# Kernel optimization log

Measured on AMD Instinct MI355X. Metric: run time of the kernel, lower is better.

The kernel has to match this reference:

```python
import jax, jax.numpy as jnp
import numpy as np

D_MODEL, N_HEADS, RANK, TOPK = 1024, 16, 32, 32
D_HEAD = D_MODEL // N_HEADS


def setup_inputs() -> dict:
    key = jax.random.key(0)
    ks = jax.random.split(key, 12)
    B, L, S = 2, 2048, 2048
    sc = 0.02
    return {
        "q": jax.random.normal(ks[0], (B, L, D_MODEL), jnp.float32),
        "k": jax.random.normal(ks[1], (B, S, D_MODEL), jnp.float32),
        "v": jax.random.normal(ks[2], (B, S, D_MODEL), jnp.float32),
        "Wq": jax.random.normal(ks[3], (D_MODEL, RANK * N_HEADS), jnp.float32) * sc,
        "bq": jnp.zeros((RANK * N_HEADS,), jnp.float32),
        "Wk": jax.random.normal(ks[4], (D_MODEL, RANK * N_HEADS), jnp.float32) * sc,
        "bk": jnp.zeros((RANK * N_HEADS,), jnp.float32),
        "Wv": jax.random.normal(ks[5], (D_MODEL, D_MODEL), jnp.float32) * sc,
        "bv": jnp.zeros((D_MODEL,), jnp.float32),
        "Wo": jax.random.normal(ks[6], (D_MODEL, D_MODEL), jnp.float32) * sc,
        "bo": jnp.zeros((D_MODEL,), jnp.float32),
        "pos_bias": jnp.zeros((1, N_HEADS, 1, 1), jnp.float32),
    }


def topk_sparse(logits, k):
    # keep top-k per row, mask the rest to -inf, then softmax
    top_vals = jax.lax.top_k(logits, k)[0]          # [B,H,L,k]
    kth = top_vals[..., -1:]                        # [B,H,L,1]
    masked = jnp.where(logits >= kth, logits, -jnp.inf)
    return jax.nn.softmax(masked, axis=-1)


def reference(q, k, v, Wq, bq, Wk, bk, Wv, bv, Wo, bo, pos_bias):
    B, L, _ = q.shape
    S = k.shape[1]
    Q = (q @ Wq + bq).reshape(B, L, N_HEADS, RANK).transpose(0, 2, 1, 3)   # [B,H,L,r]
    K = (k @ Wk + bk).reshape(B, S, N_HEADS, RANK).transpose(0, 2, 1, 3)   # [B,H,S,r]
    V = (v @ Wv + bv).reshape(B, S, N_HEADS, D_HEAD).transpose(0, 2, 1, 3)  # [B,H,S,d]
    scores = jnp.einsum('bhlr,bhsr->bhls', Q, K) / jnp.sqrt(jnp.float32(RANK))
    scores = scores + pos_bias
    attn = topk_sparse(scores, TOPK)                # [B,H,L,S]
    out = jnp.einsum('bhls,bhsd->bhld', attn, V)    # [B,H,L,d]
    out = out.transpose(0, 2, 1, 3).reshape(B, L, D_MODEL)
    return out @ Wo + bo
```

## Files before the change

kernel.cpp:

```cpp
#include <hip/hip_runtime.h>
#include <hip/hip_bf16.h>
#include <cstdint>

constexpr int B  = 2;
constexpr int L  = 2048;
constexpr int S  = 2048;
constexpr int DM = 1024;
constexpr int H  = 16;
constexpr int R  = 32;
constexpr int DH = 64;
constexpr int TOPK = 32;
constexpr int SELCAP = 36;
constexpr float SCALE = 0.17677669529663687f;


using short8 = __attribute__((ext_vector_type(8))) short;
using f32x4  = __attribute__((ext_vector_type(4))) float;

__device__ __forceinline__ unsigned short bf16_rne(float x) {
    unsigned int u = __float_as_uint(x);
    unsigned int r = u + 0x7FFFu + ((u >> 16) & 1u);
    return (unsigned short)(r >> 16);
}
__device__ __forceinline__ float bf16_up(unsigned short h) {
    return __uint_as_float((unsigned int)h << 16);
}
__device__ __forceinline__ float inv_sortable(unsigned int uu) {
    unsigned int sg2 = (unsigned int)(((int)uu) >> 31);
    return __uint_as_float(uu ^ (0x80000000u | ~sg2));
}

__global__ __launch_bounds__(256, 2)
void qk_proj(const float* __restrict__ Aq, const float* __restrict__ Wq_,
             const float* __restrict__ bq_, float* __restrict__ Qp,
             const float* __restrict__ Ak, const float* __restrict__ Wk_,
             const float* __restrict__ bk_, unsigned short* __restrict__ Kf,
             int M, int N, int K)
{
    const int z = blockIdx.z;
    const float* A    = z ? Ak  : Aq;
    const float* W    = z ? Wk_ : Wq_;
    const float* bias = z ? bk_ : bq_;

    __shared__ float As[16][136];
    __shared__ float Ws[16][132];

    const int t  = threadIdx.x;
    const int tx = t & 15;
    const int ty = t >> 4;
    const int m0 = blockIdx.y * 128;
    const int n0 = blockIdx.x * 128;

    float acc[8][8];
#pragma unroll
    for (int i = 0; i < 8; ++i)
#pragma unroll
        for (int j = 0; j < 8; ++j) acc[i][j] = 0.f;

    for (int kb = 0; kb < K; kb += 16) {
        __syncthreads();
#pragma unroll
        for (int it = 0; it < 2; ++it) {
            int f4  = t + it * 256;
            int row = f4 >> 2;
            int cg  = (f4 & 3) * 4;
            float4 av = *(const float4*)&A[(size_t)(m0 + row) * K + kb + cg];
            As[cg + 0][row] = av.x;
            As[cg + 1][row] = av.y;
            As[cg + 2][row] = av.z;
            As[cg + 3][row] = av.w;
        }
#pragma unroll
        for (int it = 0; it < 2; ++it) {
            int f4 = t + it * 256;
            int kk = f4 >> 5;
            int cb = (f4 & 31) * 4;
            *(float4*)&Ws[kk][cb] = *(const float4*)&W[(size_t)(kb + kk) * N + n0 + cb];
        }
        __syncthreads();
#pragma unroll
        for (int kk = 0; kk < 16; ++kk) {
            float4 a0 = *(const float4*)&As[kk][ty * 8];
            float4 a1 = *(const float4*)&As[kk][ty * 8 + 4];
            float4 w0 = *(const float4*)&Ws[kk][tx * 8];
            float4 w1 = *(const float4*)&Ws[kk][tx * 8 + 4];
            float a[8] = {a0.x, a0.y, a0.z, a0.w, a1.x, a1.y, a1.z, a1.w};
            float w[8] = {w0.x, w0.y, w0.z, w0.w, w1.x, w1.y, w1.z, w1.w};
#pragma unroll
            for (int i = 0; i < 8; ++i)
#pragma unroll
                for (int j = 0; j < 8; ++j)
                    acc[i][j] = fmaf(a[i], w[j], acc[i][j]);
        }
    }

    float4 b0 = *(const float4*)&bias[n0 + tx * 8];
    float4 b1 = *(const float4*)&bias[n0 + tx * 8 + 4];

    if (z == 0) {
#pragma unroll
        for (int i = 0; i < 8; ++i) {
            float4 o0 = make_float4((acc[i][0] + b0.x) * SCALE, (acc[i][1] + b0.y) * SCALE,
                                    (acc[i][2] + b0.z) * SCALE, (acc[i][3] + b0.w) * SCALE);
            float4 o1 = make_float4((acc[i][4] + b1.x) * SCALE, (acc[i][5] + b1.y) * SCALE,
                                    (acc[i][6] + b1.z) * SCALE, (acc[i][7] + b1.w) * SCALE);
            size_t off = (size_t)(m0 + ty * 8 + i) * N + n0 + tx * 8;
            *(float4*)&Qp[off]     = o0;
            *(float4*)&Qp[off + 4] = o1;
        }
    } else {
        float bb[8] = {b0.x, b0.y, b0.z, b0.w, b1.x, b1.y, b1.z, b1.w};
        const int h2 = (n0 + tx * 8) >> 5;
        const int l4 = ((n0 + tx * 8) & 31) >> 3;
#pragma unroll
        for (int i = 0; i < 8; ++i) {
            unsigned short hh[8], mm[8], ll[8];
#pragma unroll
            for (int j = 0; j < 8; ++j) {
                float x = acc[i][j] + bb[j];
                hh[j] = bf16_rne(x);
                float xr = x - bf16_up(hh[j]);
                mm[j] = bf16_rne(xr);
                ll[j] = bf16_rne(xr - bf16_up(mm[j]));
            }
            const int grow = m0 + ty * 8 + i;
            const int bat  = grow >> 11;
            const int key  = grow & 2047;
            const int T    = key >> 4;
            const int l15  = key & 15;
            const size_t base = (((size_t)(bat * H + h2) * 128 + T) * 1536)
                              + (size_t)(l4 * 16 + l15) * 8;
            ushort4 h0v = {hh[0], hh[1], hh[2], hh[3]}, h1v = {hh[4], hh[5], hh[6], hh[7]};
            ushort4 m0v = {mm[0], mm[1], mm[2], mm[3]}, m1v = {mm[4], mm[5], mm[6], mm[7]};
            ushort4 l0v = {ll[0], ll[1], ll[2], ll[3]}, l1v = {ll[4], ll[5], ll[6], ll[7]};
            *(ushort4*)&Kf[base]            = h0v;
            *(ushort4*)&Kf[base + 4]        = h1v;
            *(ushort4*)&Kf[base + 512]      = m0v;
            *(ushort4*)&Kf[base + 512 + 4]  = m1v;
            *(ushort4*)&Kf[base + 1024]     = l0v;
            *(ushort4*)&Kf[base + 1024 + 4] = l1v;
        }
    }
}

__global__ __launch_bounds__(256)
void transpose_split_dual(const float* __restrict__ Wv_, unsigned short* __restrict__ VhT,
                          unsigned short* __restrict__ VlT,
                          const float* __restrict__ Wo_, unsigned short* __restrict__ OhT,
                          unsigned short* __restrict__ OlT, int N, int K)
{
    const int z = blockIdx.z;
    const float* W = z ? Wo_ : Wv_;
    unsigned short* Th = z ? OhT : VhT;
    unsigned short* Tl = z ? OlT : VlT;

    __shared__ float tile[32][33];
    const int n0 = blockIdx.x * 32;
    const int k0 = blockIdx.y * 32;
    const int tx = threadIdx.x & 31;
    const int ty = threadIdx.x >> 5;

#pragma unroll
    for (int i = ty; i < 32; i += 8)
        tile[i][tx] = W[(size_t)(k0 + i) * N + n0 + tx];
    __syncthreads();
#pragma unroll
    for (int i = ty; i < 32; i += 8) {
        float x = tile[tx][i];
        unsigned short h = bf16_rne(x);
        float hf = bf16_up(h);
        unsigned short l = bf16_rne(x - hf);
        Th[(size_t)(n0 + i) * K + k0 + tx] = h;
        Tl[(size_t)(n0 + i) * K + k0 + tx] = l;
    }
}

__global__ __launch_bounds__(256, 1)
void gemm_mfma_split(const float* __restrict__ A, const unsigned short* __restrict__ Bh,
                     const unsigned short* __restrict__ Bl, const float* __restrict__ bias,
                     float* __restrict__ C, int M, int N, int K)
{
    constexpr int LDT = 56;
    __shared__ unsigned short Ah[128 * LDT];
    __shared__ unsigned short Al[128 * LDT];
    __shared__ unsigned short Wh[128 * LDT];
    __shared__ unsigned short Wl[128 * LDT];

    const int t    = threadIdx.x;
    const int lane = t & 63;
    const int w    = t >> 6;
    const int wr   = w >> 1;
    const int wc   = w & 1;
    const int l15  = lane & 15;
    const int l4   = lane >> 4;
    const int m0   = blockIdx.y * 128;
    const int n0   = blockIdx.x * 128;

    f32x4 acc[4][4];
#pragma unroll
    for (int m = 0; m < 4; ++m)
#pragma unroll
        for (int n = 0; n < 4; ++n) {
            f32x4 z = {0.f, 0.f, 0.f, 0.f};
            acc[m][n] = z;
        }

#pragma unroll 1
    for (int kb = 0; kb < K; kb += 32) {
        __syncthreads();
#pragma unroll
        for (int it = 0; it < 4; ++it) {
            int f   = t + it * 256;
            int row = f >> 3;
            int kg  = (f & 7) * 4;
            float4 av = *(const float4*)&A[(size_t)(m0 + row) * K + kb + kg];
            ushort4 hv, lv;
            hv.x = bf16_rne(av.x); lv.x = bf16_rne(av.x - bf16_up(hv.x));
            hv.y = bf16_rne(av.y); lv.y = bf16_rne(av.y - bf16_up(hv.y));
            hv.z = bf16_rne(av.z); lv.z = bf16_rne(av.z - bf16_up(hv.z));
            hv.w = bf16_rne(av.w); lv.w = bf16_rne(av.w - bf16_up(hv.w));
            *(ushort4*)&Ah[row * LDT + kg] = hv;
            *(ushort4*)&Al[row * LDT + kg] = lv;
            ushort4 bh4 = *(const ushort4*)&Bh[(size_t)(n0 + row) * K + kb + kg];
            ushort4 bl4 = *(const ushort4*)&Bl[(size_t)(n0 + row) * K + kb + kg];
            *(ushort4*)&Wh[row * LDT + kg] = bh4;
            *(ushort4*)&Wl[row * LDT + kg] = bl4;
        }
        __syncthreads();

        short8 ah[4], al[4], bh[4], bl[4];
#pragma unroll
        for (int m = 0; m < 4; ++m) {
            int row = wr * 64 + m * 16 + l15;
            ah[m] = *(short8*)&Ah[row * LDT + l4 * 8];
            al[m] = *(short8*)&Al[row * LDT + l4 * 8];
        }
#pragma unroll
        for (int n = 0; n < 4; ++n) {
            int col = wc * 64 + n * 16 + l15;
            bh[n] = *(short8*)&Wh[col * LDT + l4 * 8];
            bl[n] = *(short8*)&Wl[col * LDT + l4 * 8];
        }
#pragma unroll
        for (int m = 0; m < 4; ++m)
#pragma unroll
            for (int n = 0; n < 4; ++n)
                acc[m][n] = __builtin_amdgcn_mfma_f32_16x16x32_bf16(ah[m], bh[n], acc[m][n], 0, 0, 0);
#pragma unroll
        for (int m = 0; m < 4; ++m)
#pragma unroll
            for (int n = 0; n < 4; ++n)
                acc[m][n] = __builtin_amdgcn_mfma_f32_16x16x32_bf16(ah[m], bl[n], acc[m][n], 0, 0, 0);
#pragma unroll
        for (int m = 0; m < 4; ++m)
#pragma unroll
            for (int n = 0; n < 4; ++n)
                acc[m][n] = __builtin_amdgcn_mfma_f32_16x16x32_bf16(al[m], bh[n], acc[m][n], 0, 0, 0);
    }

#pragma unroll
    for (int m = 0; m < 4; ++m) {
        int row = m0 + wr * 64 + m * 16 + l4 * 4;
#pragma unroll
        for (int n = 0; n < 4; ++n) {
            int col = n0 + wc * 64 + n * 16 + l15;
            float bv = bias[col];
#pragma unroll
            for (int r = 0; r < 4; ++r)
                C[(size_t)(row + r) * N + col] = acc[m][n][r] + bv;
        }
    }
}

__global__ __launch_bounds__(1024, 1)
void score_select_gather(const float* __restrict__ Qp,
                         const unsigned short* __restrict__ Kf,
                         const float* __restrict__ Vp, float* __restrict__ Oh)
{
    constexpr int LDS_STRIDE = 2049;
    __shared__ float sclds[16][LDS_STRIDE];
    __shared__ unsigned short Qs[3][16][32];

    const int t    = threadIdx.x;
    const int lane = t & 63;
    const int wv   = t >> 6;

    const int wgid = blockIdx.x;
    const int xcd  = wgid & 7;
    const int jj   = wgid >> 3;
    const int bh_  = xcd + 8 * (jj >> 7);
    const int tile = jj & 127;
    const int b    = bh_ >> 4;
    const int h    = bh_ & 15;
    const int lbase = tile * 16;

    if (t < 512) {
        int row = t >> 5;
        int col = t & 31;
        float x = Qp[(size_t)(b * L + lbase + row) * (H * R) + h * R + col];
        unsigned short hh = bf16_rne(x);
        float xr = x - bf16_up(hh);
        unsigned short mm = bf16_rne(xr);
        unsigned short ll = bf16_rne(xr - bf16_up(mm));
        Qs[0][row][col] = hh;
        Qs[1][row][col] = mm;
        Qs[2][row][col] = ll;
    }
    __syncthreads();

    const int l15 = lane & 15;
    const int l4  = lane >> 4;

    const short8 ah = *(const short8*)&Qs[0][l15][l4 * 8];
    const short8 am = *(const short8*)&Qs[1][l15][l4 * 8];
    const short8 al = *(const short8*)&Qs[2][l15][l4 * 8];

    const unsigned short* kfb = Kf + (size_t)bh_ * 128 * 1536;

    auto LOADT = [&](int T0, short8& h0, short8& m0v, short8& l0v,
                     short8& h1, short8& m1v, short8& l1v) {
        const unsigned short* t0 = kfb + (size_t)T0 * 1536 + lane * 8;
        h0  = *(const short8*)(t0);
        m0v = *(const short8*)(t0 + 512);
        l0v = *(const short8*)(t0 + 1024);
        h1  = *(const short8*)(t0 + 1536);
        m1v = *(const short8*)(t0 + 2048);
        l1v = *(const short8*)(t0 + 2560);
    };
    auto COMPUTE = [&](const short8& bh0, const short8& bm0, const short8& bl0,
                       const short8& bh1, const short8& bm1, const short8& bl1, int p) {
        f32x4 acc0 = {0.f, 0.f, 0.f, 0.f};
        f32x4 acc1 = {0.f, 0.f, 0.f, 0.f};
        __builtin_amdgcn_s_setprio(1);
        acc0 = __builtin_amdgcn_mfma_f32_16x16x32_bf16(ah, bh0, acc0, 0, 0, 0);
        acc1 = __builtin_amdgcn_mfma_f32_16x16x32_bf16(ah, bh1, acc1, 0, 0, 0);
        acc0 = __builtin_amdgcn_mfma_f32_16x16x32_bf16(ah, bm0, acc0, 0, 0, 0);
        acc1 = __builtin_amdgcn_mfma_f32_16x16x32_bf16(ah, bm1, acc1, 0, 0, 0);
        acc0 = __builtin_amdgcn_mfma_f32_16x16x32_bf16(am, bh0, acc0, 0, 0, 0);
        acc1 = __builtin_amdgcn_mfma_f32_16x16x32_bf16(am, bh1, acc1, 0, 0, 0);
        acc0 = __builtin_amdgcn_mfma_f32_16x16x32_bf16(am, bm0, acc0, 0, 0, 0);
        acc1 = __builtin_amdgcn_mfma_f32_16x16x32_bf16(am, bm1, acc1, 0, 0, 0);
        acc0 = __builtin_amdgcn_mfma_f32_16x16x32_bf16(ah, bl0, acc0, 0, 0, 0);
        acc1 = __builtin_amdgcn_mfma_f32_16x16x32_bf16(ah, bl1, acc1, 0, 0, 0);
        acc0 = __builtin_amdgcn_mfma_f32_16x16x32_bf16(al, bh0, acc0, 0, 0, 0);
        acc1 = __builtin_amdgcn_mfma_f32_16x16x32_bf16(al, bh1, acc1, 0, 0, 0);
        __builtin_amdgcn_s_setprio(0);
        const int kc0 = wv * 128 + p * 32 + l15;
#pragma unroll
        for (int r = 0; r < 4; ++r) {
            sclds[l4 * 4 + r][kc0]      = acc0[r];
            sclds[l4 * 4 + r][kc0 + 16] = acc1[r];
        }
    };

    {
        short8 xh0, xm0, xl0, xh1, xm1, xl1;
        short8 yh0, ym0, yl0, yh1, ym1, yl1;
        LOADT(wv * 8 + 0, xh0, xm0, xl0, xh1, xm1, xl1);
        LOADT(wv * 8 + 2, yh0, ym0, yl0, yh1, ym1, yl1);
        COMPUTE(xh0, xm0, xl0, xh1, xm1, xl1, 0);
        LOADT(wv * 8 + 4, xh0, xm0, xl0, xh1, xm1, xl1);
        COMPUTE(yh0, ym0, yl0, yh1, ym1, yl1, 1);
        LOADT(wv * 8 + 6, yh0, ym0, yl0, yh1, ym1, yl1);
        COMPUTE(xh0, xm0, xl0, xh1, xm1, xl1, 2);
        COMPUTE(yh0, ym0, yl0, yh1, ym1, yl1, 3);
    }

    __syncthreads();

    const unsigned long long lanelt = (1ull << lane) - 1ull;
    {
        const int r = wv;

        unsigned int u[32];
#pragma unroll
        for (int j = 0; j < 32; ++j) {
            unsigned int bb  = __float_as_uint(sclds[r][j * 64 + lane]);
            unsigned int sgn = (unsigned int)(((int)bb) >> 31);
            u[j] = bb ^ (sgn | 0x80000000u);
        }

        unsigned int lmax = u[0];
#pragma unroll
        for (int j = 1; j < 32; ++j) lmax = lmax > u[j] ? lmax : u[j];
        unsigned int umx = lmax;
#pragma unroll
        for (int off = 32; off >= 1; off >>= 1) {
            unsigned int o = (unsigned int)__shfl_xor((int)umx, off, 64);
            umx = umx > o ? umx : o;
        }
        const float mx = inv_sortable(umx);

        unsigned int PM = 0;
        for (int bit = 31; bit >= 0; --bit) {
            unsigned int test = PM | (1u << bit);
            int c2 = (int)__popcll(__ballot(lmax >= test));
            if (c2 >= TOPK) {
                PM = test;
                if (c2 == TOPK) break;
            }
        }

        int cbase = 0;
#pragma unroll
        for (int j = 0; j < 32; ++j) {
            bool alive = (u[j] >= PM);
            unsigned long long m = __ballot(alive);
            if (alive) {
                int pos = cbase + (int)__popcll(m & lanelt);
                if (pos < 128) {
                    sclds[r][1024 + pos] = __uint_as_float(u[j]);
                    sclds[r][1280 + pos] = __uint_as_float((unsigned int)(j * 64 + lane));
                }
            }
            cbase += (int)__popcll(m);
        }
        const int Ncand = cbase;

        float dsum = 0.f;
        int   base = 0;

        if (Ncand <= 128) {
            const bool v0 = lane < Ncand;
            const bool v1 = 64 + lane < Ncand;
            const unsigned int c0 = v0 ? __float_as_uint(sclds[r][1024 + lane])      : 0u;
            const unsigned int c1 = v1 ? __float_as_uint(sclds[r][1024 + 64 + lane]) : 0u;
            const unsigned int i0 = v0 ? __float_as_uint(sclds[r][1280 + lane])      : 0u;
            const unsigned int i1 = v1 ? __float_as_uint(sclds[r][1280 + 64 + lane]) : 0u;

            unsigned int P = 0;
            for (int bit = 31; bit >= 0; --bit) {
                unsigned int test = P | (1u << bit);
                int c2 = (int)__popcll(__ballot(v0 && c0 >= test))
                       + (int)__popcll(__ballot(v1 && c1 >= test));
                if (c2 >= TOPK) {
                    P = test;
                    if (c2 == TOPK) break;
                }
            }

            {
                bool sel = v0 && (c0 >= P);
                unsigned long long m = __ballot(sel);
                if (sel) {
                    float e = __expf(inv_sortable(c0) - mx);
                    int pos = (int)__popcll(m & lanelt);
                    if (pos < SELCAP) {
                        sclds[r][pos]       = e;
                        sclds[r][512 + pos] = __uint_as_float(i0);
                    }
                    dsum += e;
                }
                base = (int)__popcll(m);
            }
            {
                bool sel = v1 && (c1 >= P);
                unsigned long long m = __ballot(sel);
                if (sel) {
                    float e = __expf(inv_sortable(c1) - mx);
                    int pos = base + (int)__popcll(m & lanelt);
                    if (pos < SELCAP) {
                        sclds[r][pos]       = e;
                        sclds[r][512 + pos] = __uint_as_float(i1);
                    }
                    dsum += e;
                }
                base += (int)__popcll(m);
            }
        } else {
            unsigned int P = 0;
            for (int bit = 31; bit >= 0; --bit) {
                unsigned int test = P | (1u << bit);
                int c2 = 0;
#pragma unroll
                for (int j = 0; j < 32; ++j)
                    c2 += (int)__popcll(__ballot(u[j] >= test));
                if (c2 >= TOPK) {
                    P = test;
                    if (c2 == TOPK) break;
                }
            }
#pragma unroll
            for (int j = 0; j < 32; ++j) {
                bool sel = (u[j] >= P);
                unsigned long long m = __ballot(sel);
                if (sel) {
                    float e = __expf(inv_sortable(u[j]) - mx);
                    int pos = base + (int)__popcll(m & lanelt);
                    if (pos < SELCAP) {
                        sclds[r][pos]       = e;
                        sclds[r][512 + pos] = __uint_as_float((unsigned int)(j * 64 + lane));
                    }
                    dsum += e;
                }
                base += (int)__popcll(m);
            }
        }
#pragma unroll
        for (int off = 32; off >= 1; off >>= 1)
            dsum += __shfl_xor(dsum, off, 64);

        const int cn = base < SELCAP ? base : SELCAP;
        const float inv = 1.0f / dsum;
        const float* vb = Vp + (size_t)b * S * DM + h * DH + lane;

        float a0 = 0.f, a1 = 0.f, a2 = 0.f, a3 = 0.f;
        float a4 = 0.f, a5 = 0.f, a6 = 0.f, a7 = 0.f;
        int tt = 0;
        for (; tt + 8 <= cn; tt += 8) {
            int   s0 = (int)__float_as_uint(sclds[r][512 + tt + 0]);
            int   s1 = (int)__float_as_uint(sclds[r][512 + tt + 1]);
            int   s2 = (int)__float_as_uint(sclds[r][512 + tt + 2]);
            int   s3 = (int)__float_as_uint(sclds[r][512 + tt + 3]);
            int   s4 = (int)__float_as_uint(sclds[r][512 + tt + 4]);
            int   s5 = (int)__float_as_uint(sclds[r][512 + tt + 5]);
            int   s6 = (int)__float_as_uint(sclds[r][512 + tt + 6]);
            int   s7 = (int)__float_as_uint(sclds[r][512 + tt + 7]);
            float w0 = sclds[r][tt + 0], w1 = sclds[r][tt + 1];
            float w2 = sclds[r][tt + 2], w3 = sclds[r][tt + 3];
            float w4 = sclds[r][tt + 4], w5 = sclds[r][tt + 5];
            float w6 = sclds[r][tt + 6], w7 = sclds[r][tt + 7];
            a0 = fmaf(w0, vb[(size_t)s0 * DM], a0);
            a1 = fmaf(w1, vb[(size_t)s1 * DM], a1);
            a2 = fmaf(w2, vb[(size_t)s2 * DM], a2);
            a3 = fmaf(w3, vb[(size_t)s3 * DM], a3);
            a4 = fmaf(w4, vb[(size_t)s4 * DM], a4);
            a5 = fmaf(w5, vb[(size_t)s5 * DM], a5);
            a6 = fmaf(w6, vb[(size_t)s6 * DM], a6);
            a7 = fmaf(w7, vb[(size_t)s7 * DM], a7);
        }
        for (; tt < cn; ++tt) {
            int s0 = (int)__float_as_uint(sclds[r][512 + tt]);
            a0 = fmaf(sclds[r][tt], vb[(size_t)s0 * DM], a0);
        }
        Oh[(size_t)(b * L + lbase + r) * DM + h * DH + lane] =
            (((a0 + a1) + (a2 + a3)) + ((a4 + a5) + (a6 + a7))) * inv;
    }
}

extern "C" void kernel_launch(void* const* d_in, const int* in_sizes, int n_in,
                              void* d_out, int out_size, void* d_ws, size_t ws_size,
                              hipStream_t stream)
{
    const float* q  = (const float*)d_in[0];
    const float* k  = (const float*)d_in[1];
    const float* v  = (const float*)d_in[2];
    const float* Wq = (const float*)d_in[3];
    const float* bq = (const float*)d_in[4];
    const float* Wk = (const float*)d_in[5];
    const float* bk = (const float*)d_in[6];
    const float* Wv = (const float*)d_in[7];
    const float* bv = (const float*)d_in[8];
    const float* Wo = (const float*)d_in[9];
    const float* bo = (const float*)d_in[10];

    float* out = (float*)d_out;
    char*  ws  = (char*)d_ws;

    const size_t MB = 1024 * 1024;
    float*          Qp = (float*)(ws);
    unsigned short* Kf = (unsigned short*)(ws + 8 * MB);
    float*          Vp = (float*)(ws + 20 * MB);
    float*          Oh = (float*)(ws + 36 * MB);
    unsigned short* WvH = (unsigned short*)(ws + 36 * MB);
    unsigned short* WvL = (unsigned short*)(ws + 38 * MB);
    unsigned short* WoH = (unsigned short*)(ws + 52 * MB);
    unsigned short* WoL = (unsigned short*)(ws + 54 * MB);

    const int M = B * L;
    dim3 blk(256);

    transpose_split_dual<<<dim3(DM / 32, DM / 32, 2), blk, 0, stream>>>(
        Wv, WvH, WvL, Wo, WoH, WoL, DM, DM);

    gemm_mfma_split<<<dim3(DM / 128, M / 128), blk, 0, stream>>>(v, WvH, WvL, bv, Vp, M, DM, DM);

    qk_proj<<<dim3((H * R) / 128, M / 128, 2), blk, 0, stream>>>(
        q, Wq, bq, Qp, k, Wk, bk, Kf, M, H * R, DM);

    score_select_gather<<<dim3(4096), dim3(1024), 0, stream>>>(Qp, Kf, Vp, Oh);

    gemm_mfma_split<<<dim3(DM / 128, M / 128), blk, 0, stream>>>(Oh, WoH, WoL, bo, out, M, DM, DM);
}
```

Before: 465.8 us.

## Pre-swizzle split weights into MFMA fragment layout and load directly from global

```diff
diff --git a/kernel.cpp b/kernel.cpp
--- a/kernel.cpp
+++ b/kernel.cpp
@@ -24,6 +24,11 @@
 }
 __device__ __forceinline__ float bf16_up(unsigned short h) {
     return __uint_as_float((unsigned int)h << 16);
+}
+__device__ __forceinline__ unsigned int to_sortable(float f) {
+    unsigned int bb  = __float_as_uint(f);
+    unsigned int sgn = (unsigned int)(((int)bb) >> 31);
+    return bb ^ (sgn | 0x80000000u);
 }
 __device__ __forceinline__ float inv_sortable(unsigned int uu) {
     unsigned int sg2 = (unsigned int)(((int)uu) >> 31);
@@ -164,14 +169,22 @@
     for (int i = ty; i < 32; i += 8)
         tile[i][tx] = W[(size_t)(k0 + i) * N + n0 + tx];
     __syncthreads();
+
+    const int kk  = k0 + tx;
+    const int c32 = kk >> 5;
+    const int l4v = (kk >> 3) & 3;
+    const int el  = kk & 7;
 #pragma unroll
     for (int i = ty; i < 32; i += 8) {
         float x = tile[tx][i];
         unsigned short h = bf16_rne(x);
         float hf = bf16_up(h);
         unsigned short l = bf16_rne(x - hf);
-        Th[(size_t)(n0 + i) * K + k0 + tx] = h;
-        Tl[(size_t)(n0 + i) * K + k0 + tx] = l;
+        const int n   = n0 + i;
+        const size_t fo = ((size_t)(n >> 4) * 32 + c32) * 512
+                        + (size_t)(l4v * 16 + (n & 15)) * 8 + el;
+        Th[fo] = h;
+        Tl[fo] = l;
     }
 }
 
@@ -182,9 +195,7 @@
 {
     constexpr int LDT = 56;
     __shared__ unsigned short Ah[128 * LDT];
-    __shared__ unsigned short Al[128 * LDT];
-    __shared__ unsigned short Wh[128 * LDT];
-    __shared__ unsigned short Wl[128 * LDT];
+    __shared__ unsigned short Al[128 * LDT + 8192];
 
     const int t    = threadIdx.x;
     const int lane = t & 63;
@@ -221,10 +232,6 @@
             hv.w = bf16_rne(av.w); lv.w = bf16_rne(av.w - bf16_up(hv.w));
             *(ushort4*)&Ah[row * LDT + kg] = hv;
             *(ushort4*)&Al[row * LDT + kg] = lv;
-            ushort4 bh4 = *(const ushort4*)&Bh[(size_t)(n0 + row) * K + kb + kg];
-            ushort4 bl4 = *(const ushort4*)&Bl[(size_t)(n0 + row) * K + kb + kg];
-            *(ushort4*)&Wh[row * LDT + kg] = bh4;
-            *(ushort4*)&Wl[row * LDT + kg] = bl4;
         }
         __syncthreads();
 
@@ -235,11 +242,13 @@
             ah[m] = *(short8*)&Ah[row * LDT + l4 * 8];
             al[m] = *(short8*)&Al[row * LDT + l4 * 8];
         }
+        const int kb32 = kb >> 5;
 #pragma unroll
         for (int n = 0; n < 4; ++n) {
-            int col = wc * 64 + n * 16 + l15;
-            bh[n] = *(short8*)&Wh[col * LDT + l4 * 8];
-            bl[n] = *(short8*)&Wl[col * LDT + l4 * 8];
+            const int T = (n0 >> 4) + wc * 4 + n;
+            const size_t fo = ((size_t)T * 32 + kb32) * 512 + (size_t)lane * 8;
+            bh[n] = *(const short8*)&Bh[fo];
+            bl[n] = *(const short8*)&Bl[fo];
         }
 #pragma unroll
         for (int m = 0; m < 4; ++m)
@@ -372,25 +381,19 @@
     {
         const int r = wv;
 
-        unsigned int u[32];
-#pragma unroll
-        for (int j = 0; j < 32; ++j) {
-            unsigned int bb  = __float_as_uint(sclds[r][j * 64 + lane]);
-            unsigned int sgn = (unsigned int)(((int)bb) >> 31);
-            u[j] = bb ^ (sgn | 0x80000000u);
-        }
-
-        unsigned int lmax = u[0];
-#pragma unroll
-        for (int j = 1; j < 32; ++j) lmax = lmax > u[j] ? lmax : u[j];
-        unsigned int umx = lmax;
-#pragma unroll
-        for (int off = 32; off >= 1; off >>= 1) {
-            unsigned int o = (unsigned int)__shfl_xor((int)umx, off, 64);
-            umx = umx > o ? umx : o;
-        }
-        const float mx = inv_sortable(umx);
-
+        float sreg[32];
+#pragma unroll
+        for (int j = 0; j < 32; ++j) sreg[j] = sclds[r][j * 64 + lane];
+
+        float lmaxf = sreg[0];
+#pragma unroll
+        for (int j = 1; j < 32; ++j) lmaxf = fmaxf(lmaxf, sreg[j]);
+        float mx = lmaxf;
+#pragma unroll
+        for (int off = 32; off >= 1; off >>= 1)
+            mx = fmaxf(mx, __shfl_xor(mx, off, 64));
+
+        const unsigned int lmax = to_sortable(lmaxf);
         unsigned int PM = 0;
         for (int bit = 31; bit >= 0; --bit) {
             unsigned int test = PM | (1u << bit);
@@ -400,16 +403,17 @@
                 if (c2 == TOPK) break;
             }
         }
+        const float TM = inv_sortable(PM);
 
         int cbase = 0;
 #pragma unroll
         for (int j = 0; j < 32; ++j) {
-            bool alive = (u[j] >= PM);
+            bool alive = (sreg[j] >= TM);
             unsigned long long m = __ballot(alive);
             if (alive) {
                 int pos = cbase + (int)__popcll(m & lanelt);
                 if (pos < 128) {
-                    sclds[r][1024 + pos] = __uint_as_float(u[j]);
+                    sclds[r][1024 + pos] = sreg[j];
                     sclds[r][1280 + pos] = __uint_as_float((unsigned int)(j * 64 + lane));
                 }
             }
@@ -423,16 +427,18 @@
         if (Ncand <= 128) {
             const bool v0 = lane < Ncand;
             const bool v1 = 64 + lane < Ncand;
-            const unsigned int c0 = v0 ? __float_as_uint(sclds[r][1024 + lane])      : 0u;
-            const unsigned int c1 = v1 ? __float_as_uint(sclds[r][1024 + 64 + lane]) : 0u;
+            const float c0f = v0 ? sclds[r][1024 + lane]      : 0.f;
+            const float c1f = v1 ? sclds[r][1024 + 64 + lane] : 0.f;
             const unsigned int i0 = v0 ? __float_as_uint(sclds[r][1280 + lane])      : 0u;
             const unsigned int i1 = v1 ? __float_as_uint(sclds[r][1280 + 64 + lane]) : 0u;
+            const unsigned int cu0 = v0 ? to_sortable(c0f) : 0u;
+            const unsigned int cu1 = v1 ? to_sortable(c1f) : 0u;
 
             unsigned int P = 0;
             for (int bit = 31; bit >= 0; --bit) {
                 unsigned int test = P | (1u << bit);
-                int c2 = (int)__popcll(__ballot(v0 && c0 >= test))
-                       + (int)__popcll(__ballot(v1 && c1 >= test));
+                int c2 = (int)__popcll(__ballot(v0 && cu0 >= test))
+                       + (int)__popcll(__ballot(v1 && cu1 >= test));
                 if (c2 >= TOPK) {
                     P = test;
                     if (c2 == TOPK) break;
@@ -440,10 +446,10 @@
             }
 
             {
-                bool sel = v0 && (c0 >= P);
+                bool sel = v0 && (cu0 >= P);
                 unsigned long long m = __ballot(sel);
                 if (sel) {
-                    float e = __expf(inv_sortable(c0) - mx);
+                    float e = __expf(c0f - mx);
                     int pos = (int)__popcll(m & lanelt);
                     if (pos < SELCAP) {
                         sclds[r][pos]       = e;
@@ -454,10 +460,10 @@
                 base = (int)__popcll(m);
             }
             {
-                bool sel = v1 && (c1 >= P);
+                bool sel = v1 && (cu1 >= P);
                 unsigned long long m = __ballot(sel);
                 if (sel) {
-                    float e = __expf(inv_sortable(c1) - mx);
+                    float e = __expf(c1f - mx);
                     int pos = base + (int)__popcll(m & lanelt);
                     if (pos < SELCAP) {
                         sclds[r][pos]       = e;
@@ -468,6 +474,9 @@
                 base += (int)__popcll(m);
             }
         } else {
+            unsigned int u[32];
+#pragma unroll
+            for (int j = 0; j < 32; ++j) u[j] = to_sortable(sreg[j]);
             unsigned int P = 0;
             for (int bit = 31; bit >= 0; --bit) {
                 unsigned int test = P | (1u << bit);
@@ -485,7 +494,7 @@
                 bool sel = (u[j] >= P);
                 unsigned long long m = __ballot(sel);
                 if (sel) {
-                    float e = __expf(inv_sortable(u[j]) - mx);
+                    float e = __expf(sreg[j] - mx);
                     int pos = base + (int)__popcll(m & lanelt);
                     if (pos < SELCAP) {
                         sclds[r][pos]       = e;
```

After: 478.4 us. 1.03x slower.
